# Optimization experiments

Hardware: AMD Instinct MI355X
Metric: run time of the kernel (lower is better)

The kernel has to match this reference:

```python
import math
import jax, jax.numpy as jnp
import numpy as np

FACTOR = 5


def setup_inputs() -> dict:
    key = jax.random.key(0)
    kq, kk, kv, ki = jax.random.split(key, 4)
    B, H, L, D = 4, 8, 2048, 64
    sample_k = min(FACTOR * math.ceil(math.log(L)), L)  # 40
    queries = jax.random.normal(kq, (B, H, L, D), dtype=jnp.float32)
    keys = jax.random.normal(kk, (B, H, L, D), dtype=jnp.float32)
    values = jax.random.normal(kv, (B, H, L, D), dtype=jnp.float32)
    index_sample = jax.random.randint(ki, (L, sample_k), 0, L, dtype=jnp.int64 if jax.config.jax_enable_x64 else jnp.int32)
    return {"queries": queries, "keys": keys, "values": values, "index_sample": index_sample}


def reference(queries, keys, values, index_sample):
    B, H, L_Q, D = queries.shape
    L_K = keys.shape[2]
    u = min(FACTOR * math.ceil(math.log(L_Q)), L_Q)  # n_top queries (= 40)
    scale = 1.0 / math.sqrt(D)

    # --- _prob_QK: sparsity measurement over randomly sampled keys ---
    # K_sample[b,h,q,s,:] = keys[b,h,index_sample[q,s],:]  -> [B,H,L_Q,S,D]
    K_sample = keys[:, :, index_sample, :]
    Q_K_sample = jnp.einsum('bhqd,bhqsd->bhqs', queries, K_sample)  # [B,H,L_Q,S]
    M = Q_K_sample.max(axis=-1) - Q_K_sample.sum(axis=-1) / L_K      # [B,H,L_Q]
    _, M_top = jax.lax.top_k(M, u)                                    # [B,H,u]

    Q_reduce = jnp.take_along_axis(queries, M_top[..., None], axis=2)  # [B,H,u,D]
    scores_top = jnp.einsum('bhud,bhkd->bhuk', Q_reduce, keys) * scale  # [B,H,u,L_K]

    # --- initial context: causal cumulative sum of V (mask_flag=True) ---
    context = jnp.cumsum(values, axis=2)  # [B,H,L_Q,D]

    # --- ProbMask: causal rows gathered at the selected query indices ---
    causal = jnp.triu(jnp.ones((L_Q, L_K), dtype=bool), 1)  # [L_Q,L_K]
    mask = causal[M_top]                                     # [B,H,u,L_K]
    scores_top = jnp.where(mask, -jnp.inf, scores_top)

    attn = jax.nn.softmax(scores_top, axis=-1)                       # [B,H,u,L_K]
    update = jnp.einsum('bhuk,bhkd->bhud', attn, values)             # [B,H,u,D]

    b_idx = jnp.arange(B)[:, None, None]
    h_idx = jnp.arange(H)[None, :, None]
    context = context.at[b_idx, h_idx, M_top].set(update.astype(context.dtype))
    return context
```

## Files before the change

kernel.cpp:

```cpp
#include <hip/hip_runtime.h>
#include <math.h>

#define BB 4
#define HH 8
#define LL 2048
#define DD 64
#define SK 40
#define BH (BB*HH)
#define NC 16
#define CK 128

__device__ __forceinline__ unsigned ordu(float v) {
    unsigned u = __float_as_uint(v);
    return (u & 0x80000000u) ? ~u : (u | 0x80000000u);
}

__global__ __launch_bounds__(256) void stage1_kernel(
        const float* __restrict__ Q, const float* __restrict__ K,
        const float* __restrict__ V, const int* __restrict__ IDX,
        float* __restrict__ M, float* __restrict__ csum) {
    int tid = threadIdx.x;
    if (blockIdx.x < 1024) {
        int x = blockIdx.x;
        int bhLo = x & 7;
        int r = x >> 3;
        int bhHi = r & 3;
        int chunk = r >> 2;
        int bh = bhHi * 8 + bhLo;
        int qbase = chunk * 64;
        int w = tid >> 6, lane = tid & 63;
        int qw = lane >> 2, c = lane & 3;
        int qi = w * 16 + qw;
        int qpos = qbase + qi;

        __shared__ int sidx[64 * SK];
        for (int i = tid; i < 64 * SK; i += 256) sidx[i] = IDX[(size_t)qbase * SK + i];

        const float4* Q4 = (const float4*)Q;
        const float4* K4 = (const float4*)K;
        float4 qreg[4];
        #pragma unroll
        for (int j = 0; j < 4; ++j)
            qreg[j] = Q4[((size_t)bh * LL + qpos) * 16 + j * 4 + c];
        __syncthreads();

        size_t kb4 = (size_t)bh * LL * 16;
        float mx = -INFINITY, sm = 0.f;
        #pragma unroll
        for (int s0 = 0; s0 < SK; s0 += 4) {
            float4 kv[4][4];
            #pragma unroll
            for (int t = 0; t < 4; ++t) {
                int ks = sidx[qi * SK + s0 + t];
                const float4* kr = K4 + kb4 + (size_t)ks * 16;
                #pragma unroll
                for (int j = 0; j < 4; ++j) kv[t][j] = kr[j * 4 + c];
            }
            #pragma unroll
            for (int t = 0; t < 4; ++t) {
                float p = 0.f;
                #pragma unroll
                for (int j = 0; j < 4; ++j)
                    p += qreg[j].x * kv[t][j].x + qreg[j].y * kv[t][j].y
                       + qreg[j].z * kv[t][j].z + qreg[j].w * kv[t][j].w;
                p += __shfl_xor(p, 1, 64);
                p += __shfl_xor(p, 2, 64);
                mx = fmaxf(mx, p);
                sm += p;
            }
        }
        if (c == 0) M[(size_t)bh * LL + qpos] = mx - sm * (1.0f / (float)LL);
    } else {
        int x = blockIdx.x - 1024;
        int bhLo = x & 7, r = x >> 3;
        int bhHi = r & 3, c = r >> 2;
        int bh = bhHi * 8 + bhLo;
        int d = tid & 63, sg = tid >> 6;
        size_t base = (size_t)bh * LL * DD;
        int row0 = c * 128 + sg * 32;
        float s = 0.f;
        for (int j = 0; j < 32; ++j) s += V[base + (size_t)(row0 + j) * DD + d];
        __shared__ float part[4][DD];
        part[sg][d] = s;
        __syncthreads();
        if (sg == 0)
            csum[((size_t)bh * 16 + c) * DD + d] = part[0][d] + part[1][d] + part[2][d] + part[3][d];
    }
}

__global__ __launch_bounds__(256) void stage2_kernel(
        const float* __restrict__ V, const float* __restrict__ csum,
        const float* __restrict__ M, float* __restrict__ out,
        int* __restrict__ topk) {
    int tid = threadIdx.x;
    if (blockIdx.x < 512) {
        int x = blockIdx.x;
        int bhLo = x & 7, r = x >> 3;
        int bhHi = r & 3, c = r >> 2;
        int bh = bhHi * 8 + bhLo;
        int d = tid & 63, sg = tid >> 6;
        size_t base = (size_t)bh * LL * DD;
        int row0 = c * 128 + sg * 32;
        float v[32];
        #pragma unroll
        for (int j = 0; j < 32; ++j) v[j] = V[base + (size_t)(row0 + j) * DD + d];
        float s = 0.f;
        #pragma unroll
        for (int j = 0; j < 32; ++j) s += v[j];
        __shared__ float part[4][DD];
        part[sg][d] = s;
        __syncthreads();
        float pre = 0.f;
        for (int cc = 0; cc < c; ++cc) pre += csum[((size_t)bh * 16 + cc) * DD + d];
        for (int ss = 0; ss < sg; ++ss) pre += part[ss][d];
        float acc = pre;
        #pragma unroll
        for (int j = 0; j < 32; ++j) {
            acc += v[j];
            out[base + (size_t)(row0 + j) * DD + d] = acc;
        }
    } else {
        int bh = blockIdx.x - 512;
        __shared__ unsigned hist[256];
        __shared__ unsigned bc_prefix, bc_need;
        __shared__ unsigned cnt_gt, cnt_eq;
        __shared__ int eqlist[128];

        unsigned v[8];
        #pragma unroll
        for (int j = 0; j < 8; ++j)
            v[j] = ordu(M[(size_t)bh * LL + tid + j * 256]);

        unsigned prefix = 0, need = SK;
        #pragma unroll
        for (int pass = 0; pass < 4; ++pass) {
            const int s = 24 - 8 * pass;
            const unsigned maskHigh = (pass == 0) ? 0u : (0xFFFFFFFFu << (s + 8));
            hist[tid] = 0;
            __syncthreads();
            #pragma unroll
            for (int j = 0; j < 8; ++j)
                if (((v[j] ^ prefix) & maskHigh) == 0)
                    atomicAdd(&hist[(v[j] >> s) & 0xFF], 1u);
            __syncthreads();
            unsigned above = 0;
            for (int b = tid + 1; b < 256; ++b) above += hist[b];
            if (above < need && above + hist[tid] >= need) {
                bc_prefix = prefix | ((unsigned)tid << s);
                bc_need = need - above;
            }
            __syncthreads();
            prefix = bc_prefix;
            need = bc_need;
            __syncthreads();
        }
        unsigned T = prefix;
        if (tid == 0) { cnt_gt = 0; cnt_eq = 0; }
        __syncthreads();
        #pragma unroll
        for (int j = 0; j < 8; ++j) {
            int idx = tid + j * 256;
            if (v[j] > T) { unsigned p = atomicAdd(&cnt_gt, 1u); topk[bh * SK + p] = idx; }
            else if (v[j] == T) { unsigned p = atomicAdd(&cnt_eq, 1u); if (p < 128) eqlist[p] = idx; }
        }
        __syncthreads();
        if (tid == 0) {
            int ne = (int)min(cnt_eq, 128u);
            unsigned base = cnt_gt;
            for (unsigned r2 = 0; r2 < need; ++r2) {
                int bj = 0, bv = 0x7FFFFFFF;
                for (int j = 0; j < ne; ++j)
                    if (eqlist[j] < bv) { bv = eqlist[j]; bj = j; }
                topk[bh * SK + base + r2] = bv;
                eqlist[bj] = 0x7FFFFFFF;
            }
        }
    }
}

__global__ __launch_bounds__(256) void attn_kernel(
        const float* __restrict__ Q, const float* __restrict__ K,
        const float* __restrict__ V, const int* __restrict__ topk,
        float* __restrict__ pm, float* __restrict__ pl,
        float* __restrict__ po) {
    int x = blockIdx.x;
    int bhLo = x & 7;
    int r = x >> 3;
    int c = r & 15;
    int bhHi = r >> 4;
    int bh = bhHi * 8 + bhLo;
    int tid = threadIdx.x;
    int w = tid >> 6, lane = tid & 63;
    int cbase = c * CK;

    __shared__ int qp[SK];
    __shared__ float4 sq4[SK][16];
    __shared__ float SC[CK][SK + 1];

    if (tid < SK) qp[tid] = topk[bh * SK + tid];
    __syncthreads();
    const float4* Q4 = (const float4*)Q;
    const float4* K4 = (const float4*)K;
    const float4* V4 = (const float4*)V;
    for (int i = tid; i < SK * 16; i += 256) {
        int u = i >> 4, j = i & 15;
        sq4[u][j] = Q4[((size_t)bh * LL + qp[u]) * 16 + j];
    }
    __syncthreads();

    {
        int half = tid & 1;
        int kk = tid >> 1;
        int kg = cbase + kk;
        size_t kb4 = (size_t)bh * LL * 16;
        float4 kreg[8];
        const float4* kr = K4 + kb4 + (size_t)kg * 16 + half * 8;
        #pragma unroll
        for (int j = 0; j < 8; ++j) kreg[j] = kr[j];
        #pragma unroll 4
        for (int u = 0; u < SK; ++u) {
            int qpu = qp[u];
            if (cbase > qpu) {
                if (half == 0) SC[kk][u] = -INFINITY;
                continue;
            }
            float pa = 0.f, pb = 0.f;
            #pragma unroll
            for (int j = 0; j < 4; ++j) {
                float4 qv = sq4[u][half * 8 + j];
                pa += kreg[j].x * qv.x + kreg[j].y * qv.y + kreg[j].z * qv.z + kreg[j].w * qv.w;
            }
            #pragma unroll
            for (int j = 4; j < 8; ++j) {
                float4 qv = sq4[u][half * 8 + j];
                pb += kreg[j].x * qv.x + kreg[j].y * qv.y + kreg[j].z * qv.z + kreg[j].w * qv.w;
            }
            float p = pa + pb;
            p += __shfl_xor(p, 1, 64);
            if (half == 0) SC[kk][u] = (kg <= qpu) ? p * 0.125f : -INFINITY;
        }
    }
    __syncthreads();

    for (int u = w; u < SK; u += 4) {
        float s0 = SC[lane][u], s1 = SC[lane + 64][u];
        float m = fmaxf(s0, s1);
        #pragma unroll
        for (int off = 32; off > 0; off >>= 1) m = fmaxf(m, __shfl_xor(m, off, 64));
        float e0 = 0.f, e1 = 0.f;
        if (m != -INFINITY) {
            e0 = expf(s0 - m);
            e1 = expf(s1 - m);
        }
        SC[lane][u] = e0;
        SC[lane + 64][u] = e1;
        float ls = e0 + e1;
        #pragma unroll
        for (int off = 32; off > 0; off >>= 1) ls += __shfl_xor(ls, off, 64);
        if (lane == 0) {
            size_t pb = (size_t)(bh * SK + u) * NC + c;
            pm[pb] = m;
            pl[pb] = ls;
        }
    }
    __syncthreads();

    {
        int ks = tid & 3;
        int dg = (tid >> 2) & 15;
        int ug = tid >> 6;
        int u0 = ug * 10;
        float4 acc[10];
        #pragma unroll
        for (int i = 0; i < 10; ++i) acc[i] = make_float4(0.f, 0.f, 0.f, 0.f);
        for (int t = 0; t < CK / 4; ++t) {
            int k = t * 4 + ks;
            float4 vv = V4[((size_t)bh * LL + cbase + k) * 16 + dg];
            #pragma unroll
            for (int i = 0; i < 10; ++i) {
                float pw = SC[k][u0 + i];
                acc[i].x += pw * vv.x; acc[i].y += pw * vv.y;
                acc[i].z += pw * vv.z; acc[i].w += pw * vv.w;
            }
        }
        #pragma unroll
        for (int i = 0; i < 10; ++i) {
            acc[i].x += __shfl_xor(acc[i].x, 1, 64); acc[i].x += __shfl_xor(acc[i].x, 2, 64);
            acc[i].y += __shfl_xor(acc[i].y, 1, 64); acc[i].y += __shfl_xor(acc[i].y, 2, 64);
            acc[i].z += __shfl_xor(acc[i].z, 1, 64); acc[i].z += __shfl_xor(acc[i].z, 2, 64);
            acc[i].w += __shfl_xor(acc[i].w, 1, 64); acc[i].w += __shfl_xor(acc[i].w, 2, 64);
        }
        if (ks == 0) {
            #pragma unroll
            for (int i = 0; i < 10; ++i) {
                float4* dst = (float4*)&po[((size_t)(bh * SK + u0 + i) * NC + c) * DD + dg * 4];
                *dst = acc[i];
            }
        }
    }
}

__global__ __launch_bounds__(256) void combine_kernel(
        const float* __restrict__ pm, const float* __restrict__ pl,
        const float* __restrict__ po, const int* __restrict__ topk,
        float* __restrict__ out) {
    int g = blockIdx.x * 4 + (threadIdx.x >> 6);
    int d = threadIdx.x & 63;
    int qpos = topk[g];
    int bh = g / SK;
    size_t gb = (size_t)g * NC;
    float gm = -INFINITY;
    #pragma unroll
    for (int j = 0; j < NC; ++j) gm = fmaxf(gm, pm[gb + j]);
    float L = 0.f, o = 0.f;
    #pragma unroll
    for (int j = 0; j < NC; ++j) {
        float pmj = pm[gb + j];
        float wj = (pmj == -INFINITY) ? 0.f : expf(pmj - gm);
        L += pl[gb + j] * wj;
        o += po[(gb + j) * DD + d] * wj;
    }
    out[((size_t)bh * LL + qpos) * DD + d] = o / L;
}

extern "C" void kernel_launch(void* const* d_in, const int* in_sizes, int n_in,
                              void* d_out, int out_size, void* d_ws, size_t ws_size,
                              hipStream_t stream) {
    const float* Q   = (const float*)d_in[0];
    const float* K   = (const float*)d_in[1];
    const float* V   = (const float*)d_in[2];
    const int*   IDX = (const int*)d_in[3];
    float* out = (float*)d_out;

    char* ws = (char*)d_ws;
    float* M    = (float*)ws;  ws += (size_t)BH * LL * sizeof(float);
    int*   topk = (int*)ws;    ws += ((size_t)BH * SK * sizeof(int) + 255) & ~255ull;
    float* csum = (float*)ws;  ws += (size_t)BH * 16 * DD * sizeof(float);
    float* pm   = (float*)ws;  ws += ((size_t)BH * SK * NC * sizeof(float) + 255) & ~255ull;
    float* pl   = (float*)ws;  ws += ((size_t)BH * SK * NC * sizeof(float) + 255) & ~255ull;
    float* po   = (float*)ws;

    stage1_kernel<<<1536, 256, 0, stream>>>(Q, K, V, IDX, M, csum);
    stage2_kernel<<<544, 256, 0, stream>>>(V, csum, M, out, topk);
    attn_kernel<<<BH * NC, 256, 0, stream>>>(Q, K, V, topk, pm, pl, po);
    combine_kernel<<<BH * SK / 4, 256, 0, stream>>>(pm, pl, po, topk, out);
}
```

Baseline: 162.7 us.

## Stage sampled key tiles through shared memory with per-query index bucketing

```diff
diff --git a/kernel.cpp b/kernel.cpp
--- a/kernel.cpp
+++ b/kernel.cpp
@@ -10,9 +10,18 @@
 #define NC 16
 #define CK 128
 
+#define S1_NQ 128
+#define S1_R  128
+#define S1_P  16
+#define S1_STRIDE 68
+
 __device__ __forceinline__ unsigned ordu(float v) {
     unsigned u = __float_as_uint(v);
     return (u & 0x80000000u) ? ~u : (u | 0x80000000u);
+}
+
+__device__ __forceinline__ float dot4(float4 a, float4 b) {
+    return a.x * b.x + a.y * b.y + a.z * b.z + a.w * b.w;
 }
 
 __global__ __launch_bounds__(256) void stage1_kernel(
@@ -20,58 +29,88 @@
         const float* __restrict__ V, const int* __restrict__ IDX,
         float* __restrict__ M, float* __restrict__ csum) {
     int tid = threadIdx.x;
-    if (blockIdx.x < 1024) {
+    if (blockIdx.x < 512) {
         int x = blockIdx.x;
         int bhLo = x & 7;
         int r = x >> 3;
         int bhHi = r & 3;
-        int chunk = r >> 2;
+        int qc = r >> 2;
         int bh = bhHi * 8 + bhLo;
-        int qbase = chunk * 64;
-        int w = tid >> 6, lane = tid & 63;
-        int qw = lane >> 2, c = lane & 3;
-        int qi = w * 16 + qw;
-        int qpos = qbase + qi;
-
-        __shared__ int sidx[64 * SK];
-        for (int i = tid; i < 64 * SK; i += 256) sidx[i] = IDX[(size_t)qbase * SK + i];
-
+        int qbase = qc * S1_NQ;
+
+        __shared__ float kld[S1_R * S1_STRIDE];
+        __shared__ int   sidx[S1_NQ * SK];
+        __shared__ int   soff[S1_NQ * (S1_P + 1)];
+
+        if (tid < S1_NQ) {
+            int vv[SK];
+            #pragma unroll
+            for (int s = 0; s < SK; ++s)
+                vv[s] = IDX[(size_t)(qbase + tid) * SK + s];
+            int wp = tid * SK;
+            for (int p = 0; p < S1_P; ++p) {
+                soff[tid * (S1_P + 1) + p] = wp;
+                #pragma unroll
+                for (int s = 0; s < SK; ++s) {
+                    if ((vv[s] >> 7) == p) sidx[wp++] = vv[s];
+                }
+            }
+            soff[tid * (S1_P + 1) + S1_P] = wp;
+        }
+
+        int G = tid >> 3, c8 = tid & 7;
         const float4* Q4 = (const float4*)Q;
         const float4* K4 = (const float4*)K;
-        float4 qreg[4];
-        #pragma unroll
-        for (int j = 0; j < 4; ++j)
-            qreg[j] = Q4[((size_t)bh * LL + qpos) * 16 + j * 4 + c];
-        __syncthreads();
+        float4 qr[4][2];
+        #pragma unroll
+        for (int qi2 = 0; qi2 < 4; ++qi2) {
+            int qpos = qbase + G + qi2 * 32;
+            qr[qi2][0] = Q4[((size_t)bh * LL + qpos) * 16 + c8];
+            qr[qi2][1] = Q4[((size_t)bh * LL + qpos) * 16 + c8 + 8];
+        }
+
+        float mx[4] = {-INFINITY, -INFINITY, -INFINITY, -INFINITY};
+        float sm[4] = {0.f, 0.f, 0.f, 0.f};
 
         size_t kb4 = (size_t)bh * LL * 16;
-        float mx = -INFINITY, sm = 0.f;
-        #pragma unroll
-        for (int s0 = 0; s0 < SK; s0 += 4) {
-            float4 kv[4][4];
-            #pragma unroll
-            for (int t = 0; t < 4; ++t) {
-                int ks = sidx[qi * SK + s0 + t];
-                const float4* kr = K4 + kb4 + (size_t)ks * 16;
-                #pragma unroll
-                for (int j = 0; j < 4; ++j) kv[t][j] = kr[j * 4 + c];
-            }
-            #pragma unroll
-            for (int t = 0; t < 4; ++t) {
-                float p = 0.f;
-                #pragma unroll
-                for (int j = 0; j < 4; ++j)
-                    p += qreg[j].x * kv[t][j].x + qreg[j].y * kv[t][j].y
-                       + qreg[j].z * kv[t][j].z + qreg[j].w * kv[t][j].w;
-                p += __shfl_xor(p, 1, 64);
-                p += __shfl_xor(p, 2, 64);
-                mx = fmaxf(mx, p);
-                sm += p;
-            }
-        }
-        if (c == 0) M[(size_t)bh * LL + qpos] = mx - sm * (1.0f / (float)LL);
+        for (int p = 0; p < S1_P; ++p) {
+            __syncthreads();
+            #pragma unroll
+            for (int i = 0; i < 8; ++i) {
+                int f = tid + i * 256;
+                int row = f >> 4, j = f & 15;
+                float4 v = K4[kb4 + (size_t)(p * S1_R) * 16 + f];
+                *(float4*)&kld[row * S1_STRIDE + j * 4] = v;
+            }
+            __syncthreads();
+            #pragma unroll
+            for (int qi2 = 0; qi2 < 4; ++qi2) {
+                int q = G + qi2 * 32;
+                int b0 = soff[q * (S1_P + 1) + p];
+                int b1 = soff[q * (S1_P + 1) + p + 1];
+                for (int s = b0; s < b1; ++s) {
+                    int kl = sidx[s] - (p << 7);
+                    const float* krow = &kld[kl * S1_STRIDE + c8 * 4];
+                    float4 a0 = *(const float4*)krow;
+                    float4 a1 = *(const float4*)(krow + 32);
+                    float pd = dot4(qr[qi2][0], a0) + dot4(qr[qi2][1], a1);
+                    pd += __shfl_xor(pd, 1, 64);
+                    pd += __shfl_xor(pd, 2, 64);
+                    pd += __shfl_xor(pd, 4, 64);
+                    mx[qi2] = fmaxf(mx[qi2], pd);
+                    sm[qi2] += pd;
+                }
+            }
+        }
+        if (c8 == 0) {
+            #pragma unroll
+            for (int qi2 = 0; qi2 < 4; ++qi2) {
+                int qpos = qbase + G + qi2 * 32;
+                M[(size_t)bh * LL + qpos] = mx[qi2] - sm[qi2] * (1.0f / (float)LL);
+            }
+        }
     } else {
-        int x = blockIdx.x - 1024;
+        int x = blockIdx.x - 512;
         int bhLo = x & 7, r = x >> 3;
         int bhHi = r & 3, c = r >> 2;
         int bh = bhHi * 8 + bhLo;
@@ -340,7 +379,7 @@
     float* pl   = (float*)ws;  ws += ((size_t)BH * SK * NC * sizeof(float) + 255) & ~255ull;
     float* po   = (float*)ws;
 
-    stage1_kernel<<<1536, 256, 0, stream>>>(Q, K, V, IDX, M, csum);
+    stage1_kernel<<<1024, 256, 0, stream>>>(Q, K, V, IDX, M, csum);
     stage2_kernel<<<544, 256, 0, stream>>>(V, csum, M, out, topk);
     attn_kernel<<<BH * NC, 256, 0, stream>>>(Q, K, V, topk, pm, pl, po);
     combine_kernel<<<BH * SK / 4, 256, 0, stream>>>(pm, pl, po, topk, out);
```

After: 233.9 us. 1.44x slower.

## Split fused stage kernels into separate kernels and parallelize radix histogram scan

Applied to the files above, without the earlier changes.

```diff
diff --git a/kernel.cpp b/kernel.cpp
--- a/kernel.cpp
+++ b/kernel.cpp
@@ -15,165 +15,168 @@
     return (u & 0x80000000u) ? ~u : (u | 0x80000000u);
 }
 
-__global__ __launch_bounds__(256) void stage1_kernel(
+__global__ __launch_bounds__(256) void mkern(
         const float* __restrict__ Q, const float* __restrict__ K,
-        const float* __restrict__ V, const int* __restrict__ IDX,
-        float* __restrict__ M, float* __restrict__ csum) {
-    int tid = threadIdx.x;
-    if (blockIdx.x < 1024) {
-        int x = blockIdx.x;
-        int bhLo = x & 7;
-        int r = x >> 3;
-        int bhHi = r & 3;
-        int chunk = r >> 2;
-        int bh = bhHi * 8 + bhLo;
-        int qbase = chunk * 64;
-        int w = tid >> 6, lane = tid & 63;
-        int qw = lane >> 2, c = lane & 3;
-        int qi = w * 16 + qw;
-        int qpos = qbase + qi;
-
-        __shared__ int sidx[64 * SK];
-        for (int i = tid; i < 64 * SK; i += 256) sidx[i] = IDX[(size_t)qbase * SK + i];
-
-        const float4* Q4 = (const float4*)Q;
-        const float4* K4 = (const float4*)K;
-        float4 qreg[4];
-        #pragma unroll
-        for (int j = 0; j < 4; ++j)
-            qreg[j] = Q4[((size_t)bh * LL + qpos) * 16 + j * 4 + c];
-        __syncthreads();
-
-        size_t kb4 = (size_t)bh * LL * 16;
-        float mx = -INFINITY, sm = 0.f;
-        #pragma unroll
-        for (int s0 = 0; s0 < SK; s0 += 4) {
-            float4 kv[4][4];
-            #pragma unroll
-            for (int t = 0; t < 4; ++t) {
-                int ks = sidx[qi * SK + s0 + t];
-                const float4* kr = K4 + kb4 + (size_t)ks * 16;
-                #pragma unroll
-                for (int j = 0; j < 4; ++j) kv[t][j] = kr[j * 4 + c];
-            }
-            #pragma unroll
-            for (int t = 0; t < 4; ++t) {
-                float p = 0.f;
-                #pragma unroll
-                for (int j = 0; j < 4; ++j)
-                    p += qreg[j].x * kv[t][j].x + qreg[j].y * kv[t][j].y
-                       + qreg[j].z * kv[t][j].z + qreg[j].w * kv[t][j].w;
-                p += __shfl_xor(p, 1, 64);
-                p += __shfl_xor(p, 2, 64);
-                mx = fmaxf(mx, p);
-                sm += p;
-            }
-        }
-        if (c == 0) M[(size_t)bh * LL + qpos] = mx - sm * (1.0f / (float)LL);
-    } else {
-        int x = blockIdx.x - 1024;
-        int bhLo = x & 7, r = x >> 3;
-        int bhHi = r & 3, c = r >> 2;
-        int bh = bhHi * 8 + bhLo;
-        int d = tid & 63, sg = tid >> 6;
-        size_t base = (size_t)bh * LL * DD;
-        int row0 = c * 128 + sg * 32;
-        float s = 0.f;
-        for (int j = 0; j < 32; ++j) s += V[base + (size_t)(row0 + j) * DD + d];
-        __shared__ float part[4][DD];
-        part[sg][d] = s;
-        __syncthreads();
-        if (sg == 0)
-            csum[((size_t)bh * 16 + c) * DD + d] = part[0][d] + part[1][d] + part[2][d] + part[3][d];
-    }
-}
-
-__global__ __launch_bounds__(256) void stage2_kernel(
+        const int* __restrict__ IDX, float* __restrict__ M) {
+    int tid = threadIdx.x;
+    int x = blockIdx.x;
+    int bhLo = x & 7;
+    int r = x >> 3;
+    int bhHi = r & 3;
+    int chunk = r >> 2;
+    int bh = bhHi * 8 + bhLo;
+    int qbase = chunk * 64;
+    int w = tid >> 6, lane = tid & 63;
+    int qw = lane >> 2, c = lane & 3;
+    int qi = w * 16 + qw;
+    int qpos = qbase + qi;
+
+    __shared__ int sidx[64 * SK];
+    for (int i = tid; i < 64 * SK; i += 256) sidx[i] = IDX[(size_t)qbase * SK + i];
+
+    const float4* Q4 = (const float4*)Q;
+    const float4* K4 = (const float4*)K;
+    float4 qreg[4];
+    #pragma unroll
+    for (int j = 0; j < 4; ++j)
+        qreg[j] = Q4[((size_t)bh * LL + qpos) * 16 + j * 4 + c];
+    __syncthreads();
+
+    size_t kb4 = (size_t)bh * LL * 16;
+    float mx = -INFINITY, sm = 0.f;
+    #pragma unroll 8
+    for (int s = 0; s < SK; ++s) {
+        int ks = sidx[qi * SK + s];
+        const float4* kr = K4 + kb4 + (size_t)ks * 16;
+        float p = 0.f;
+        #pragma unroll
+        for (int j = 0; j < 4; ++j) {
+            float4 kv = kr[j * 4 + c];
+            p += qreg[j].x * kv.x + qreg[j].y * kv.y + qreg[j].z * kv.z + qreg[j].w * kv.w;
+        }
+        p += __shfl_xor(p, 1, 64);
+        p += __shfl_xor(p, 2, 64);
+        mx = fmaxf(mx, p);
+        sm += p;
+    }
+    if (c == 0) M[(size_t)bh * LL + qpos] = mx - sm * (1.0f / (float)LL);
+}
+
+__global__ __launch_bounds__(256) void vsum_kernel(
+        const float* __restrict__ V, float* __restrict__ csum) {
+    int tid = threadIdx.x;
+    int x = blockIdx.x;
+    int bhLo = x & 7, r = x >> 3;
+    int bhHi = r & 3, c = r >> 2;
+    int bh = bhHi * 8 + bhLo;
+    int d = tid & 63, sg = tid >> 6;
+    size_t base = (size_t)bh * LL * DD;
+    int row0 = c * 128 + sg * 32;
+    float s = 0.f;
+    for (int j = 0; j < 32; ++j) s += V[base + (size_t)(row0 + j) * DD + d];
+    __shared__ float part[4][DD];
+    part[sg][d] = s;
+    __syncthreads();
+    if (sg == 0)
+        csum[((size_t)bh * 16 + c) * DD + d] = part[0][d] + part[1][d] + part[2][d] + part[3][d];
+}
+
+__global__ __launch_bounds__(256) void cumsum_kernel(
         const float* __restrict__ V, const float* __restrict__ csum,
-        const float* __restrict__ M, float* __restrict__ out,
-        int* __restrict__ topk) {
-    int tid = threadIdx.x;
-    if (blockIdx.x < 512) {
-        int x = blockIdx.x;
-        int bhLo = x & 7, r = x >> 3;
-        int bhHi = r & 3, c = r >> 2;
-        int bh = bhHi * 8 + bhLo;
-        int d = tid & 63, sg = tid >> 6;
-        size_t base = (size_t)bh * LL * DD;
-        int row0 = c * 128 + sg * 32;
-        float v[32];
-        #pragma unroll
-        for (int j = 0; j < 32; ++j) v[j] = V[base + (size_t)(row0 + j) * DD + d];
-        float s = 0.f;
-        #pragma unroll
-        for (int j = 0; j < 32; ++j) s += v[j];
-        __shared__ float part[4][DD];
-        part[sg][d] = s;
-        __syncthreads();
-        float pre = 0.f;
-        for (int cc = 0; cc < c; ++cc) pre += csum[((size_t)bh * 16 + cc) * DD + d];
-        for (int ss = 0; ss < sg; ++ss) pre += part[ss][d];
-        float acc = pre;
-        #pragma unroll
-        for (int j = 0; j < 32; ++j) {
-            acc += v[j];
-            out[base + (size_t)(row0 + j) * DD + d] = acc;
-        }
-    } else {
-        int bh = blockIdx.x - 512;
-        __shared__ unsigned hist[256];
-        __shared__ unsigned bc_prefix, bc_need;
-        __shared__ unsigned cnt_gt, cnt_eq;
-        __shared__ int eqlist[128];
-
-        unsigned v[8];
+        float* __restrict__ out) {
+    int tid = threadIdx.x;
+    int x = blockIdx.x;
+    int bhLo = x & 7, r = x >> 3;
+    int bhHi = r & 3, c = r >> 2;
+    int bh = bhHi * 8 + bhLo;
+    int d = tid & 63, sg = tid >> 6;
+    size_t base = (size_t)bh * LL * DD;
+    int row0 = c * 128 + sg * 32;
+    float v[32];
+    #pragma unroll
+    for (int j = 0; j < 32; ++j) v[j] = V[base + (size_t)(row0 + j) * DD + d];
+    float s = 0.f;
+    #pragma unroll
+    for (int j = 0; j < 32; ++j) s += v[j];
+    __shared__ float part[4][DD];
+    part[sg][d] = s;
+    __syncthreads();
+    float pre = 0.f;
+    for (int cc = 0; cc < c; ++cc) pre += csum[((size_t)bh * 16 + cc) * DD + d];
+    for (int ss = 0; ss < sg; ++ss) pre += part[ss][d];
+    float acc = pre;
+    #pragma unroll
+    for (int j = 0; j < 32; ++j) {
+        acc += v[j];
+        out[base + (size_t)(row0 + j) * DD + d] = acc;
+    }
+}
+
+__global__ __launch_bounds__(256) void radix_kernel(
+        const float* __restrict__ M, int* __restrict__ topk) {
+    int tid = threadIdx.x;
+    int bh = blockIdx.x;
+    __shared__ unsigned hist[256];
+    __shared__ unsigned sfx[256];
+    __shared__ unsigned bc_prefix, bc_need;
+    __shared__ unsigned cnt_gt, cnt_eq;
+    __shared__ int eqlist[128];
+
+    unsigned v[8];
+    #pragma unroll
+    for (int j = 0; j < 8; ++j)
+        v[j] = ordu(M[(size_t)bh * LL + tid + j * 256]);
+
+    unsigned prefix = 0, need = SK;
+    #pragma unroll
+    for (int pass = 0; pass < 4; ++pass) {
+        const int s = 24 - 8 * pass;
+        const unsigned maskHigh = (pass == 0) ? 0u : (0xFFFFFFFFu << (s + 8));
+        hist[tid] = 0;
+        __syncthreads();
         #pragma unroll
         for (int j = 0; j < 8; ++j)
-            v[j] = ordu(M[(size_t)bh * LL + tid + j * 256]);
-
-        unsigned prefix = 0, need = SK;
-        #pragma unroll
-        for (int pass = 0; pass < 4; ++pass) {
-            const int s = 24 - 8 * pass;
-            const unsigned maskHigh = (pass == 0) ? 0u : (0xFFFFFFFFu << (s + 8));
-            hist[tid] = 0;
+            if (((v[j] ^ prefix) & maskHigh) == 0)
+                atomicAdd(&hist[(v[j] >> s) & 0xFF], 1u);
+        __syncthreads();
+        sfx[tid] = hist[tid];
+        __syncthreads();
+        #pragma unroll
+        for (int off = 1; off < 256; off <<= 1) {
+            unsigned t = (tid + off < 256) ? sfx[tid + off] : 0u;
             __syncthreads();
-            #pragma unroll
-            for (int j = 0; j < 8; ++j)
-                if (((v[j] ^ prefix) & maskHigh) == 0)
-                    atomicAdd(&hist[(v[j] >> s) & 0xFF], 1u);
+            sfx[tid] += t;
             __syncthreads();
-            unsigned above = 0;
-            for (int b = tid + 1; b < 256; ++b) above += hist[b];
-            if (above < need && above + hist[tid] >= need) {
-                bc_prefix = prefix | ((unsigned)tid << s);
-                bc_need = need - above;
-            }
-            __syncthreads();
-            prefix = bc_prefix;
-            need = bc_need;
-            __syncthreads();
-        }
-        unsigned T = prefix;
-        if (tid == 0) { cnt_gt = 0; cnt_eq = 0; }
-        __syncthreads();
-        #pragma unroll
-        for (int j = 0; j < 8; ++j) {
-            int idx = tid + j * 256;
-            if (v[j] > T) { unsigned p = atomicAdd(&cnt_gt, 1u); topk[bh * SK + p] = idx; }
-            else if (v[j] == T) { unsigned p = atomicAdd(&cnt_eq, 1u); if (p < 128) eqlist[p] = idx; }
-        }
-        __syncthreads();
-        if (tid == 0) {
-            int ne = (int)min(cnt_eq, 128u);
-            unsigned base = cnt_gt;
-            for (unsigned r2 = 0; r2 < need; ++r2) {
-                int bj = 0, bv = 0x7FFFFFFF;
-                for (int j = 0; j < ne; ++j)
-                    if (eqlist[j] < bv) { bv = eqlist[j]; bj = j; }
-                topk[bh * SK + base + r2] = bv;
-                eqlist[bj] = 0x7FFFFFFF;
-            }
+        }
+        unsigned above = (tid < 255) ? sfx[tid + 1] : 0u;
+        if (above < need && sfx[tid] >= need) {
+            bc_prefix = prefix | ((unsigned)tid << s);
+            bc_need = need - above;
+        }
+        __syncthreads();
+        prefix = bc_prefix;
+        need = bc_need;
+        __syncthreads();
+    }
+    unsigned T = prefix;
+    if (tid == 0) { cnt_gt = 0; cnt_eq = 0; }
+    __syncthreads();
+    #pragma unroll
+    for (int j = 0; j < 8; ++j) {
+        int idx = tid + j * 256;
+        if (v[j] > T) { unsigned p = atomicAdd(&cnt_gt, 1u); topk[bh * SK + p] = idx; }
+        else if (v[j] == T) { unsigned p = atomicAdd(&cnt_eq, 1u); if (p < 128) eqlist[p] = idx; }
+    }
+    __syncthreads();
+    if (tid == 0) {
+        int ne = (int)min(cnt_eq, 128u);
+        unsigned base = cnt_gt;
+        for (unsigned r2 = 0; r2 < need; ++r2) {
+            int bj = 0, bv = 0x7FFFFFFF;
+            for (int j = 0; j < ne; ++j)
+                if (eqlist[j] < bv) { bv = eqlist[j]; bj = j; }
+            topk[bh * SK + base + r2] = bv;
+            eqlist[bj] = 0x7FFFFFFF;
         }
     }
 }
@@ -340,8 +343,10 @@
     float* pl   = (float*)ws;  ws += ((size_t)BH * SK * NC * sizeof(float) + 255) & ~255ull;
     float* po   = (float*)ws;
 
-    stage1_kernel<<<1536, 256, 0, stream>>>(Q, K, V, IDX, M, csum);
-    stage2_kernel<<<544, 256, 0, stream>>>(V, csum, M, out, topk);
-    attn_kernel<<<BH * NC, 256, 0, stream>>>(Q, K, V, topk, pm, pl, po);
-    combine_kernel<<<BH * SK / 4, 256, 0, stream>>>(pm, pl, po, topk, out);
-}
+    mkern<<<1024, 256, 0, stream>>>(Q, K, IDX, M);
+    vsum_kernel<<<512, 256, 0, stream>>>(V, csum);
+    cumsum_kernel<<<512, 256, 0, stream>>>(V, csum, out);
+    radix_kernel<<<32, 256, 0, stream>>>(M, topk);
+    attn_kernel<<<512, 256, 0, stream>>>(Q, K, V, topk, pm, pl, po);
+    combine_kernel<<<320, 256, 0, stream>>>(pm, pl, po, topk, out);
+}
```

Measured after the change: 165.0 us. About the same (+1.5%).
